# Kernel optimization log

Measured on AMD Instinct MI355X. Metric: run time of the kernel, lower is better.

The kernel has to match this reference:

```python
import jax, jax.numpy as jnp
import numpy as np

CHUNK = 256
THETA = 10000.0

def rope2d(x):
    # x: (b, h, n, d), d divisible by 4
    b, h, n, d = x.shape
    pad = (-n) % CHUNK
    if pad:
        x = jnp.pad(x, ((0, 0), (0, 0), (0, pad), (0, 0)))
    c = (n + pad) // CHUNK
    x = x.reshape(b, h, c, CHUNK, d)
    inv = 1.0 / THETA ** (jnp.arange(0, d, 4, dtype=jnp.float32) / d)  # (d/4,)
    fl = jnp.arange(CHUNK, dtype=jnp.float32)[:, None] * inv[None, :]  # (l, d/4)
    cos_l, sin_l = jnp.cos(fl), jnp.sin(fl)
    fc = jnp.arange(c, dtype=jnp.float32)[:, None] * inv[None, :]      # (c, d/4)
    cos_c, sin_c = jnp.cos(fc)[:, None, :], jnp.sin(fc)[:, None, :]    # (c, 1, d/4)
    x1, x2, x3, x4 = jnp.split(x, 4, axis=-1)
    r1 = x1 * cos_l - x2 * sin_l
    r2 = x1 * sin_l + x2 * cos_l
    r3 = x3 * cos_c - x4 * sin_c
    r4 = x3 * sin_c + x4 * cos_c
    out = jnp.concatenate([r1, r2, r3, r4], axis=-1).reshape(b, h, c * CHUNK, d)
    return out[:, :, :n]


def setup_inputs():
    key = jax.random.key(0)
    ks = jax.random.split(key, 6)
    dim, heads = 512, 8
    b, n = 2, 2048
    s = 0.02
    return {
        'x': jax.random.normal(ks[0], (b, n, dim), dtype=jnp.float32),
        'w_qkv': jax.random.normal(ks[1], (3 * dim, dim), dtype=jnp.float32) * s,
        'b_qkv': jnp.zeros((3 * dim,), dtype=jnp.float32),
        'w_pre': jax.random.normal(ks[2], (heads, heads), dtype=jnp.float32) * 0.3,
        'w_post': jax.random.normal(ks[3], (heads, heads), dtype=jnp.float32) * 0.3,
        'w_out': jax.random.normal(ks[4], (dim, dim), dtype=jnp.float32) * s,
        'b_out': jnp.zeros((dim,), dtype=jnp.float32),
    }


def reference(x, w_qkv, b_qkv, w_pre, w_post, w_out, b_out):
    b, n, dim = x.shape
    heads = w_pre.shape[0]
    d = dim // heads
    scale = d ** -0.5
    qkv = x @ w_qkv.T + b_qkv                      # (b, n, 3*dim)
    q, k, v = jnp.split(qkv, 3, axis=-1)
    def to_heads(t):
        return t.reshape(b, n, heads, d).transpose(0, 2, 1, 3)  # (b, h, n, d)
    q, k, v = to_heads(q), to_heads(k), to_heads(v)
    q = rope2d(q)
    k = rope2d(k)
    logits = jnp.einsum('bhid,bhjd->bhij', q, k) * scale
    # talking-heads pre-softmax mix (Linear over head dim, no bias)
    logits = jnp.einsum('bhij,gh->bgij', logits, w_pre)
    attn = jax.nn.softmax(logits, axis=-1)
    # post-softmax mix
    attn = jnp.einsum('bhij,gh->bgij', attn, w_post)
    out = jnp.einsum('bhij,bhjd->bhid', attn, v)   # (b, h, n, d)
    out = out.transpose(0, 2, 1, 3).reshape(b, n, dim)
    return out @ w_out.T + b_out
```

## Files before the change

kernel.cpp:

```cpp
#include <hip/hip_runtime.h>
#include <hip/hip_bf16.h>

typedef __attribute__((ext_vector_type(8))) short bf16x8;
typedef __attribute__((ext_vector_type(4))) float f32x4;

#define DEV static __device__ __forceinline__

DEV unsigned short f2bf(float f) {
    __hip_bfloat16 h = __float2bfloat16(f);
    return __builtin_bit_cast(unsigned short, h);
}
DEV float bf2f(unsigned short s) {
    union { unsigned int u; float f; } v; v.u = ((unsigned int)s) << 16; return v.f;
}
DEV bf16x8 ld_bf8(const unsigned short* p) { return *reinterpret_cast<const bf16x8*>(p); }
DEV f32x4 mfma16(bf16x8 a, bf16x8 b, f32x4 c) {
    return __builtin_amdgcn_mfma_f32_16x16x32_bf16(a, b, c, 0, 0, 0);
}
DEV bf16x8 make_wfrag(const float* wmat, int li, int lg, float scale) {
    bf16x8 f = {};
    if (lg == 0 && li < 8) {
        #pragma unroll
        for (int t = 0; t < 8; t++) f[t] = (short)f2bf(wmat[li*8 + t] * scale);
    }
    return f;
}

__global__ __launch_bounds__(256) void k_qkv(
    const float* __restrict__ xf, const float* __restrict__ wf,
    const float* __restrict__ bias,
    unsigned short* __restrict__ Qb, unsigned short* __restrict__ Kb,
    unsigned short* __restrict__ Vt)
{
    __shared__ unsigned short As[64][40];
    __shared__ unsigned short Bs[64][40];
    const int m0 = blockIdx.x * 64, c0 = blockIdx.y * 64;
    const int t = threadIdx.x;
    const int w = t >> 6, lane = t & 63, li = lane & 15, lg = lane >> 4;
    const int wr = w >> 1, wc = w & 1;
    f32x4 acc[2][2] = {};
    const int srow = t >> 2, spart = (t & 3) * 8;
    for (int kt = 0; kt < 512; kt += 32) {
        const float* xs = &xf[(size_t)(m0 + srow) * 512 + kt + spart];
        float4 a0 = *(const float4*)xs, a1 = *(const float4*)(xs + 4);
        const float* wsrc = &wf[(size_t)(c0 + srow) * 512 + kt + spart];
        float4 b0 = *(const float4*)wsrc, b1 = *(const float4*)(wsrc + 4);
        ushort4 ua0 = { f2bf(a0.x), f2bf(a0.y), f2bf(a0.z), f2bf(a0.w) };
        ushort4 ua1 = { f2bf(a1.x), f2bf(a1.y), f2bf(a1.z), f2bf(a1.w) };
        ushort4 ub0 = { f2bf(b0.x), f2bf(b0.y), f2bf(b0.z), f2bf(b0.w) };
        ushort4 ub1 = { f2bf(b1.x), f2bf(b1.y), f2bf(b1.z), f2bf(b1.w) };
        *(ushort4*)&As[srow][spart] = ua0; *(ushort4*)&As[srow][spart + 4] = ua1;
        *(ushort4*)&Bs[srow][spart] = ub0; *(ushort4*)&Bs[srow][spart + 4] = ub1;
        __syncthreads();
        bf16x8 af[2], bfr[2];
        #pragma unroll
        for (int mf = 0; mf < 2; mf++) af[mf] = ld_bf8(&As[wr*32 + mf*16 + li][lg*8]);
        #pragma unroll
        for (int nf = 0; nf < 2; nf++) bfr[nf] = ld_bf8(&Bs[wc*32 + nf*16 + li][lg*8]);
        #pragma unroll
        for (int mf = 0; mf < 2; mf++)
            #pragma unroll
            for (int nf = 0; nf < 2; nf++)
                acc[mf][nf] = mfma16(af[mf], bfr[nf], acc[mf][nf]);
        __syncthreads();
    }
    const int type = c0 >> 9;
    const int head = (c0 & 511) >> 6;
    const float b0s = bias[c0 + wc*32 + li];
    const float b1s = bias[c0 + wc*32 + 16 + li];
    float invf = 0.f;
    if (type < 2) invf = powf(10000.f, -(float)li * (1.f/16.f));
    #pragma unroll
    for (int mf = 0; mf < 2; mf++) {
        #pragma unroll
        for (int r = 0; r < 4; r++) {
            int grow = m0 + wr*32 + mf*16 + lg*4 + r;
            int tok = grow & 2047, bb = grow >> 11;
            float v0 = acc[mf][0][r] + b0s;
            float v1 = acc[mf][1][r] + b1s;
            if (type < 2) {
                float ang = (wc == 0 ? (float)(tok & 255) : (float)(tok >> 8)) * invf;
                float s, c;
                sincosf(ang, &s, &c);
                float r0 = v0 * c - v1 * s;
                float r1 = v0 * s + v1 * c;
                unsigned short* dst = (type == 0 ? Qb : Kb);
                size_t base = (((size_t)(bb*8 + head)) * 2048 + tok) * 64 + wc*32 + li;
                dst[base]      = f2bf(r0);
                dst[base + 16] = f2bf(r1);
            } else {
                size_t base = (((size_t)(bb*8 + head)) * 64 + wc*32 + li) * 2048 + tok;
                Vt[base]             = f2bf(v0);
                Vt[base + 16 * 2048] = f2bf(v1);
            }
        }
    }
}

#define JC(x) (jh*1024 + ((x) > 15 ? 15 : (x))*64)

#define LOADK(JX) do { const int j0_ = (JX); \
    _Pragma("unroll") for (int nf = 0; nf < 4; nf++) { \
        const unsigned short* kp_ = Kp + (size_t)(j0_ + nf*16 + li) * 64; \
        kf[nf*2]   = ld_bf8(kp_ + lg*8); \
        kf[nf*2+1] = ld_bf8(kp_ + 32 + lg*8); } \
} while (0)

#define LOADV(JX) do { const int j0_ = (JX); \
    _Pragma("unroll") for (int nf = 0; nf < 4; nf++) { \
        const unsigned short* vp_ = Vp + (size_t)(nf*16 + li) * 2048 + j0_; \
        vf[nf*2]   = ld_bf8(vp_ + lg*8); \
        vf[nf*2+1] = ld_bf8(vp_ + 32 + lg*8); } \
} while (0)

#define QKW(LTW) do { \
    f32x4 sq0 = {}, sq1 = {}, sq2 = {}, sq3 = {}; \
    sq0 = mfma16(qa0, kf[0], sq0); sq0 = mfma16(qa1, kf[1], sq0); \
    sq1 = mfma16(qa0, kf[2], sq1); sq1 = mfma16(qa1, kf[3], sq1); \
    sq2 = mfma16(qa0, kf[4], sq2); sq2 = mfma16(qa1, kf[5], sq2); \
    sq3 = mfma16(qa0, kf[6], sq3); sq3 = mfma16(qa1, kf[7], sq3); \
    _Pragma("unroll") for (int r = 0; r < 4; r++) { \
        LTW[((lg*4 + r)*64 +  0 + li)*8 + w] = f2bf(sq0[r]); \
        LTW[((lg*4 + r)*64 + 16 + li)*8 + w] = f2bf(sq1[r]); \
        LTW[((lg*4 + r)*64 + 32 + li)*8 + w] = f2bf(sq2[r]); \
        LTW[((lg*4 + r)*64 + 48 + li)*8 + w] = f2bf(sq3[r]); } \
} while (0)

#define MIX(LTR) do { \
    _Pragma("unroll") for (int x = 0; x < 2; x++) { \
        const int i2 = 2*w + x; f32x4 invl = x ? invlB : invlA; \
        _Pragma("unroll") for (int jj = 0; jj < 4; jj++) { \
            const int e0 = i2*64 + jj*16; \
            bf16x8 bfv = {}; \
            if (lg == 0) bfv = *(const bf16x8*)&LTR[(e0 + li)*8]; \
            f32x4 d = mfma16(W1f, bfv, zero); \
            float p0 = exp2f(d[0]) * invl[0], p1 = exp2f(d[1]) * invl[1]; \
            float p2 = exp2f(d[2]) * invl[2], p3 = exp2f(d[3]) * invl[3]; \
            unsigned lo = (unsigned)f2bf(p0) | ((unsigned)f2bf(p1) << 16); \
            unsigned hi = (unsigned)f2bf(p2) | ((unsigned)f2bf(p3) << 16); \
            unsigned plo = (unsigned)__shfl_xor((int)lo, 16); \
            unsigned phi = (unsigned)__shfl_xor((int)hi, 16); \
            union { unsigned u[4]; bf16x8 v; } af_; \
            af_.u[0] = lo; af_.u[1] = hi; af_.u[2] = plo; af_.u[3] = phi; \
            f32x4 a2 = mfma16(af_.v, W2f, zero); \
            if (li < 8) { \
                ushort4 o = { f2bf(a2[0]), f2bf(a2[1]), f2bf(a2[2]), f2bf(a2[3]) }; \
                *(ushort4*)&Ah[li*1168 + i2*72 + jj*16 + lg*4] = o; } \
        } } \
} while (0)

#define PVOP() do { \
    _Pragma("unroll") for (int kk = 0; kk < 2; kk++) { \
        bf16x8 pa = *(const bf16x8*)&Ah[w*1168 + li*72 + kk*32 + lg*8]; \
        oacc[0] = mfma16(pa, vf[0 + kk], oacc[0]); \
        oacc[1] = mfma16(pa, vf[2 + kk], oacc[1]); \
        oacc[2] = mfma16(pa, vf[4 + kk], oacc[2]); \
        oacc[3] = mfma16(pa, vf[6 + kk], oacc[3]); } \
} while (0)

#define SUMEXP(LTR) do { \
    _Pragma("unroll") for (int x = 0; x < 2; x++) { \
        const int i2 = 2*w + x; float s_ = 0.f; \
        _Pragma("unroll") for (int jj = 0; jj < 4; jj++) { \
            const int e0 = i2*64 + jj*16; \
            bf16x8 bfv = {}; \
            if (lg == 0) bfv = *(const bf16x8*)&LTR[(e0 + li)*8]; \
            f32x4 d = mfma16(bfv, W1f, zero); \
            s_ += (exp2f(d[0]) + exp2f(d[1])) + (exp2f(d[2]) + exp2f(d[3])); } \
        if (x == 0) lacc0 += s_; else lacc1 += s_; } \
} while (0)

__global__ __launch_bounds__(512, 4) void k_lsum(
    const unsigned short* __restrict__ Qb, const unsigned short* __restrict__ Kb,
    const float* __restrict__ w_pre, float* __restrict__ Lp)
{
    __shared__ unsigned short LtA[8192];
    __shared__ unsigned short LtB[8192];
    const int orig = blockIdx.x;
    const int virt = ((orig & 7) << 6) | (orig >> 3);
    const int jh = virt & 1, it = (virt >> 1) & 127, bb = virt >> 8;
    const int i0 = it * 16;
    const int tid = threadIdx.x, w = tid >> 6, lane = tid & 63, li = lane & 15, lg = lane >> 4;
    bf16x8 W1f = make_wfrag(w_pre, li, lg, 0.125f * 1.44269504088896340736f);
    const unsigned short* Qp = Qb + (((size_t)(bb*8 + w)) * 2048 + i0 + li) * 64;
    bf16x8 qa0 = ld_bf8(Qp + lg*8), qa1 = ld_bf8(Qp + 32 + lg*8);
    const unsigned short* Kp = Kb + ((size_t)(bb*8 + w)) * 2048 * 64;
    const f32x4 zero = {};
    bf16x8 kf[8];
    LOADK(JC(0));
    QKW(LtA);
    LOADK(JC(1));
    __syncthreads();
    float lacc0 = 0.f, lacc1 = 0.f;
    #pragma unroll 1
    for (int tt = 0; tt < 8; tt++) {
        QKW(LtB);
        SUMEXP(LtA);
        LOADK(JC(2*tt + 2));
        __syncthreads();
        if (tt < 7) { QKW(LtA); }
        SUMEXP(LtB);
        if (tt < 7) { LOADK(JC(2*tt + 3)); }
        __syncthreads();
    }
    lacc0 += __shfl_xor(lacc0, 16); lacc0 += __shfl_xor(lacc0, 32);
    lacc1 += __shfl_xor(lacc1, 16); lacc1 += __shfl_xor(lacc1, 32);
    if (lg == 0 && li < 8) {
        float* Lpw = Lp + (size_t)jh * 32768;
        size_t base = (size_t)bb*2048 + i0;
        Lpw[(base + 2*w + 0)*8 + li] = lacc0;
        Lpw[(base + 2*w + 1)*8 + li] = lacc1;
    }
}

__global__ __launch_bounds__(512, 4) void k_attn(
    const unsigned short* __restrict__ Qb, const unsigned short* __restrict__ Kb,
    const unsigned short* __restrict__ Vt,
    const float* __restrict__ w_pre, const float* __restrict__ w_post,
    const float* __restrict__ Lp,
    unsigned short* __restrict__ AOp0, unsigned short* __restrict__ AOp1)
{
    __shared__ unsigned short LtA[8192];
    __shared__ unsigned short LtB[8192];
    __shared__ unsigned short Ah[8 * 1168];
    __shared__ float Llds[128];
    const int orig = blockIdx.x;
    const int virt = ((orig & 7) << 6) | (orig >> 3);
    const int jh = virt & 1, it = (virt >> 1) & 127, bb = virt >> 8;
    const int i0 = it * 16;
    const int tid = threadIdx.x, w = tid >> 6, lane = tid & 63, li = lane & 15, lg = lane >> 4;
    bf16x8 W1f = make_wfrag(w_pre, li, lg, 0.125f * 1.44269504088896340736f);
    bf16x8 W2f = make_wfrag(w_post, li, lg, 1.0f);
    if (tid < 128) {
        size_t g = ((size_t)bb*2048 + i0 + (tid >> 3)) * 8 + (tid & 7);
        Llds[tid] = 1.0f / (Lp[g] + Lp[32768 + g]);
    }
    const unsigned short* Qp = Qb + (((size_t)(bb*8 + w)) * 2048 + i0 + li) * 64;
    bf16x8 qa0 = ld_bf8(Qp + lg*8), qa1 = ld_bf8(Qp + 32 + lg*8);
    const unsigned short* Kp = Kb + ((size_t)(bb*8 + w)) * 2048 * 64;
    const unsigned short* Vp = Vt + ((size_t)(bb*8 + w)) * 64 * 2048;
    const f32x4 zero = {};
    bf16x8 kf[8], vf[8];
    LOADK(JC(0));
    LOADV(JC(0));
    QKW(LtA);
    LOADK(JC(1));
    __syncthreads();
    const int lgc = lg & 1;
    f32x4 invlA = *(const f32x4*)&Llds[(2*w + 0)*8 + lgc*4];
    f32x4 invlB = *(const f32x4*)&Llds[(2*w + 1)*8 + lgc*4];
    f32x4 oacc[4] = {};
    #pragma unroll 1
    for (int tt = 0; tt < 8; tt++) {
        QKW(LtB);
        MIX(LtA);
        __syncthreads();
        PVOP();
        LOADV(JC(2*tt + 1));
        LOADK(JC(2*tt + 2));
        __syncthreads();
        if (tt < 7) { QKW(LtA); }
        MIX(LtB);
        __syncthreads();
        PVOP();
        if (tt < 7) { LOADV(JC(2*tt + 2)); LOADK(JC(2*tt + 3)); }
        __syncthreads();
    }
    unsigned short* ao = jh ? AOp1 : AOp0;
    #pragma unroll
    for (int nf = 0; nf < 4; nf++)
        #pragma unroll
        for (int r = 0; r < 4; r++)
            ao[((size_t)bb*2048 + i0 + lg*4 + r)*512 + w*64 + nf*16 + li] = f2bf(oacc[nf][r]);
}

__global__ __launch_bounds__(256) void k_out(
    const unsigned short* __restrict__ a0, const unsigned short* __restrict__ a1,
    const float* __restrict__ wf, const float* __restrict__ bias,
    float* __restrict__ out)
{
    __shared__ unsigned short As[64][40];
    __shared__ unsigned short Bs[64][40];
    const int m0 = blockIdx.x * 64, c0 = blockIdx.y * 64;
    const int t = threadIdx.x;
    const int w = t >> 6, lane = t & 63, li = lane & 15, lg = lane >> 4;
    const int wr = w >> 1, wc = w & 1;
    f32x4 acc[2][2] = {};
    const int srow = t >> 2, spart = (t & 3) * 8;
    for (int kt = 0; kt < 512; kt += 32) {
        size_t aidx = (size_t)(m0 + srow) * 512 + kt + spart;
        uint4 ua = *(const uint4*)&a0[aidx];
        uint4 ub = *(const uint4*)&a1[aidx];
        const unsigned short* pa = (const unsigned short*)&ua;
        const unsigned short* pb = (const unsigned short*)&ub;
        unsigned short us[8];
        #pragma unroll
        for (int q = 0; q < 8; q++) us[q] = f2bf(bf2f(pa[q]) + bf2f(pb[q]));
        *reinterpret_cast<uint4*>(&As[srow][spart]) = *(const uint4*)us;
        const float* wsrc = &wf[(size_t)(c0 + srow) * 512 + kt + spart];
        float4 b0 = *(const float4*)wsrc, b1 = *(const float4*)(wsrc + 4);
        ushort4 ub0 = { f2bf(b0.x), f2bf(b0.y), f2bf(b0.z), f2bf(b0.w) };
        ushort4 ub1 = { f2bf(b1.x), f2bf(b1.y), f2bf(b1.z), f2bf(b1.w) };
        *(ushort4*)&Bs[srow][spart] = ub0; *(ushort4*)&Bs[srow][spart + 4] = ub1;
        __syncthreads();
        bf16x8 af[2], bfr[2];
        #pragma unroll
        for (int mf = 0; mf < 2; mf++) af[mf] = ld_bf8(&As[wr*32 + mf*16 + li][lg*8]);
        #pragma unroll
        for (int nf = 0; nf < 2; nf++) bfr[nf] = ld_bf8(&Bs[wc*32 + nf*16 + li][lg*8]);
        #pragma unroll
        for (int mf = 0; mf < 2; mf++)
            #pragma unroll
            for (int nf = 0; nf < 2; nf++)
                acc[mf][nf] = mfma16(af[mf], bfr[nf], acc[mf][nf]);
        __syncthreads();
    }
    #pragma unroll
    for (int mf = 0; mf < 2; mf++)
        #pragma unroll
        for (int nf = 0; nf < 2; nf++)
            #pragma unroll
            for (int r = 0; r < 4; r++) {
                int grow = m0 + wr*32 + mf*16 + lg*4 + r;
                int gcol = c0 + wc*32 + nf*16 + li;
                out[(size_t)grow * 512 + gcol] = acc[mf][nf][r] + bias[gcol];
            }
}

extern "C" void kernel_launch(void* const* d_in, const int* in_sizes, int n_in,
                              void* d_out, int out_size, void* d_ws, size_t ws_size,
                              hipStream_t stream)
{
    const float* x      = (const float*)d_in[0];
    const float* w_qkv  = (const float*)d_in[1];
    const float* b_qkv  = (const float*)d_in[2];
    const float* w_pre  = (const float*)d_in[3];
    const float* w_post = (const float*)d_in[4];
    const float* w_out  = (const float*)d_in[5];
    const float* b_out  = (const float*)d_in[6];
    float* out = (float*)d_out;

    char* ws = (char*)d_ws;
    unsigned short* Qb   = (unsigned short*)(ws);
    unsigned short* Kb   = (unsigned short*)(ws + 4194304);
    unsigned short* Vt   = (unsigned short*)(ws + 8388608);
    unsigned short* AOp0 = (unsigned short*)(ws + 12582912);
    unsigned short* AOp1 = (unsigned short*)(ws + 16777216);
    float* Lp            = (float*)(ws + 20971520);

    k_qkv<<<dim3(64, 24), 256, 0, stream>>>(x, w_qkv, b_qkv, Qb, Kb, Vt);
    k_lsum<<<512, 512, 0, stream>>>(Qb, Kb, w_pre, Lp);
    k_attn<<<512, 512, 0, stream>>>(Qb, Kb, Vt, w_pre, w_post, Lp, AOp0, AOp1);
    k_out<<<dim3(64, 8), 256, 0, stream>>>(AOp0, AOp1, w_out, b_out, out);
}
```

Measured before the change: 271.3 us.

## Compute all heads per wave and do talking-heads mixing in registers

Reorganizes k_lsum and k_attn so each wave computes QK logits for all 8 heads over its own 16-key slice, with Q staged in LDS. The pre- and post-softmax head mixes then run as scalar FMAs in registers instead of through LDS transposes and small MFMAs. The softmax normalizer becomes a log-sum subtracted inside exp2. This removes the per-element LDS scatter and shuffle traffic of the previous mixing path. In exchange it adds many scalar FMAs per logit, and K/V fragment loads are no longer software-prefetched.

```diff
diff --git a/kernel.cpp b/kernel.cpp
--- a/kernel.cpp
+++ b/kernel.cpp
@@ -16,14 +16,6 @@
 DEV bf16x8 ld_bf8(const unsigned short* p) { return *reinterpret_cast<const bf16x8*>(p); }
 DEV f32x4 mfma16(bf16x8 a, bf16x8 b, f32x4 c) {
     return __builtin_amdgcn_mfma_f32_16x16x32_bf16(a, b, c, 0, 0, 0);
-}
-DEV bf16x8 make_wfrag(const float* wmat, int li, int lg, float scale) {
-    bf16x8 f = {};
-    if (lg == 0 && li < 8) {
-        #pragma unroll
-        for (int t = 0; t < 8; t++) f[t] = (short)f2bf(wmat[li*8 + t] * scale);
-    }
-    return f;
 }
 
 __global__ __launch_bounds__(256) void k_qkv(
@@ -97,119 +89,79 @@
     }
 }
 
-#define JC(x) (jh*1024 + ((x) > 15 ? 15 : (x))*64)
-
-#define LOADK(JX) do { const int j0_ = (JX); \
-    _Pragma("unroll") for (int nf = 0; nf < 4; nf++) { \
-        const unsigned short* kp_ = Kp + (size_t)(j0_ + nf*16 + li) * 64; \
-        kf[nf*2]   = ld_bf8(kp_ + lg*8); \
-        kf[nf*2+1] = ld_bf8(kp_ + 32 + lg*8); } \
+#define SCALE_L2E (0.125f * 1.44269504088896340736f)
+
+#define STAGE_Q() do { \
+    for (int v = threadIdx.x; v < 1024; v += 512) { \
+        int h_ = v >> 7, rest_ = v & 127, i_ = rest_ >> 3, ch_ = rest_ & 7; \
+        *(uint4*)&Qlds[h_][i_][ch_*8] = \
+            *(const uint4*)&Qb[(((size_t)(bb*8 + h_))*2048 + i0 + i_)*64 + ch_*8]; \
+    } \
 } while (0)
 
-#define LOADV(JX) do { const int j0_ = (JX); \
-    _Pragma("unroll") for (int nf = 0; nf < 4; nf++) { \
-        const unsigned short* vp_ = Vp + (size_t)(nf*16 + li) * 2048 + j0_; \
-        vf[nf*2]   = ld_bf8(vp_ + lg*8); \
-        vf[nf*2+1] = ld_bf8(vp_ + 32 + lg*8); } \
-} while (0)
-
-#define QKW(LTW) do { \
-    f32x4 sq0 = {}, sq1 = {}, sq2 = {}, sq3 = {}; \
-    sq0 = mfma16(qa0, kf[0], sq0); sq0 = mfma16(qa1, kf[1], sq0); \
-    sq1 = mfma16(qa0, kf[2], sq1); sq1 = mfma16(qa1, kf[3], sq1); \
-    sq2 = mfma16(qa0, kf[4], sq2); sq2 = mfma16(qa1, kf[5], sq2); \
-    sq3 = mfma16(qa0, kf[6], sq3); sq3 = mfma16(qa1, kf[7], sq3); \
-    _Pragma("unroll") for (int r = 0; r < 4; r++) { \
-        LTW[((lg*4 + r)*64 +  0 + li)*8 + w] = f2bf(sq0[r]); \
-        LTW[((lg*4 + r)*64 + 16 + li)*8 + w] = f2bf(sq1[r]); \
-        LTW[((lg*4 + r)*64 + 32 + li)*8 + w] = f2bf(sq2[r]); \
-        LTW[((lg*4 + r)*64 + 48 + li)*8 + w] = f2bf(sq3[r]); } \
-} while (0)
-
-#define MIX(LTR) do { \
-    _Pragma("unroll") for (int x = 0; x < 2; x++) { \
-        const int i2 = 2*w + x; f32x4 invl = x ? invlB : invlA; \
-        _Pragma("unroll") for (int jj = 0; jj < 4; jj++) { \
-            const int e0 = i2*64 + jj*16; \
-            bf16x8 bfv = {}; \
-            if (lg == 0) bfv = *(const bf16x8*)&LTR[(e0 + li)*8]; \
-            f32x4 d = mfma16(W1f, bfv, zero); \
-            float p0 = exp2f(d[0]) * invl[0], p1 = exp2f(d[1]) * invl[1]; \
-            float p2 = exp2f(d[2]) * invl[2], p3 = exp2f(d[3]) * invl[3]; \
-            unsigned lo = (unsigned)f2bf(p0) | ((unsigned)f2bf(p1) << 16); \
-            unsigned hi = (unsigned)f2bf(p2) | ((unsigned)f2bf(p3) << 16); \
-            unsigned plo = (unsigned)__shfl_xor((int)lo, 16); \
-            unsigned phi = (unsigned)__shfl_xor((int)hi, 16); \
-            union { unsigned u[4]; bf16x8 v; } af_; \
-            af_.u[0] = lo; af_.u[1] = hi; af_.u[2] = plo; af_.u[3] = phi; \
-            f32x4 a2 = mfma16(af_.v, W2f, zero); \
-            if (li < 8) { \
-                ushort4 o = { f2bf(a2[0]), f2bf(a2[1]), f2bf(a2[2]), f2bf(a2[3]) }; \
-                *(ushort4*)&Ah[li*1168 + i2*72 + jj*16 + lg*4] = o; } \
-        } } \
-} while (0)
-
-#define PVOP() do { \
-    _Pragma("unroll") for (int kk = 0; kk < 2; kk++) { \
-        bf16x8 pa = *(const bf16x8*)&Ah[w*1168 + li*72 + kk*32 + lg*8]; \
-        oacc[0] = mfma16(pa, vf[0 + kk], oacc[0]); \
-        oacc[1] = mfma16(pa, vf[2 + kk], oacc[1]); \
-        oacc[2] = mfma16(pa, vf[4 + kk], oacc[2]); \
-        oacc[3] = mfma16(pa, vf[6 + kk], oacc[3]); } \
-} while (0)
-
-#define SUMEXP(LTR) do { \
-    _Pragma("unroll") for (int x = 0; x < 2; x++) { \
-        const int i2 = 2*w + x; float s_ = 0.f; \
-        _Pragma("unroll") for (int jj = 0; jj < 4; jj++) { \
-            const int e0 = i2*64 + jj*16; \
-            bf16x8 bfv = {}; \
-            if (lg == 0) bfv = *(const bf16x8*)&LTR[(e0 + li)*8]; \
-            f32x4 d = mfma16(bfv, W1f, zero); \
-            s_ += (exp2f(d[0]) + exp2f(d[1])) + (exp2f(d[2]) + exp2f(d[3])); } \
-        if (x == 0) lacc0 += s_; else lacc1 += s_; } \
+#define QK_ALLH() do { \
+    _Pragma("unroll") for (int h = 0; h < 8; h++) { \
+        const unsigned short* kp_ = Kb + (((size_t)(bb*8 + h))*2048 + js + li)*64; \
+        bf16x8 k0_ = ld_bf8(kp_ + lg*8), k1_ = ld_bf8(kp_ + 32 + lg*8); \
+        bf16x8 q0_ = ld_bf8(&Qlds[h][li][lg*8]); \
+        bf16x8 q1_ = ld_bf8(&Qlds[h][li][32 + lg*8]); \
+        f32x4 z_ = {}; \
+        z_ = mfma16(q0_, k0_, z_); \
+        acc[h] = mfma16(q1_, k1_, z_); \
+    } \
 } while (0)
 
 __global__ __launch_bounds__(512, 4) void k_lsum(
     const unsigned short* __restrict__ Qb, const unsigned short* __restrict__ Kb,
     const float* __restrict__ w_pre, float* __restrict__ Lp)
 {
-    __shared__ unsigned short LtA[8192];
-    __shared__ unsigned short LtB[8192];
+    __shared__ unsigned short Qlds[8][16][72];
+    __shared__ float Red[8][128];
     const int orig = blockIdx.x;
     const int virt = ((orig & 7) << 6) | (orig >> 3);
     const int jh = virt & 1, it = (virt >> 1) & 127, bb = virt >> 8;
     const int i0 = it * 16;
     const int tid = threadIdx.x, w = tid >> 6, lane = tid & 63, li = lane & 15, lg = lane >> 4;
-    bf16x8 W1f = make_wfrag(w_pre, li, lg, 0.125f * 1.44269504088896340736f);
-    const unsigned short* Qp = Qb + (((size_t)(bb*8 + w)) * 2048 + i0 + li) * 64;
-    bf16x8 qa0 = ld_bf8(Qp + lg*8), qa1 = ld_bf8(Qp + 32 + lg*8);
-    const unsigned short* Kp = Kb + ((size_t)(bb*8 + w)) * 2048 * 64;
-    const f32x4 zero = {};
-    bf16x8 kf[8];
-    LOADK(JC(0));
-    QKW(LtA);
-    LOADK(JC(1));
+    STAGE_Q();
     __syncthreads();
-    float lacc0 = 0.f, lacc1 = 0.f;
+    float lacc[4][8] = {};
     #pragma unroll 1
-    for (int tt = 0; tt < 8; tt++) {
-        QKW(LtB);
-        SUMEXP(LtA);
-        LOADK(JC(2*tt + 2));
-        __syncthreads();
-        if (tt < 7) { QKW(LtA); }
-        SUMEXP(LtB);
-        if (tt < 7) { LOADK(JC(2*tt + 3)); }
-        __syncthreads();
-    }
-    lacc0 += __shfl_xor(lacc0, 16); lacc0 += __shfl_xor(lacc0, 32);
-    lacc1 += __shfl_xor(lacc1, 16); lacc1 += __shfl_xor(lacc1, 32);
-    if (lg == 0 && li < 8) {
+    for (int s = 0; s < 8; s++) {
+        const int js = jh*1024 + s*128 + w*16;
+        f32x4 acc[8];
+        QK_ALLH();
+        #pragma unroll
+        for (int r = 0; r < 4; r++) {
+            #pragma unroll
+            for (int a = 0; a < 8; a++) {
+                float t = 0.f;
+                #pragma unroll
+                for (int h = 0; h < 8; h++) t = fmaf(w_pre[a*8 + h], acc[h][r], t);
+                lacc[r][a] += __builtin_amdgcn_exp2f(t * SCALE_L2E);
+            }
+        }
+    }
+    #pragma unroll
+    for (int m = 1; m <= 8; m <<= 1)
+        #pragma unroll
+        for (int r = 0; r < 4; r++)
+            #pragma unroll
+            for (int a = 0; a < 8; a++)
+                lacc[r][a] += __shfl_xor(lacc[r][a], m);
+    if (li == 0) {
+        #pragma unroll
+        for (int r = 0; r < 4; r++)
+            #pragma unroll
+            for (int a = 0; a < 8; a++)
+                Red[w][(lg*4 + r)*8 + a] = lacc[r][a];
+    }
+    __syncthreads();
+    if (tid < 128) {
+        float s = 0.f;
+        #pragma unroll
+        for (int ww = 0; ww < 8; ww++) s += Red[ww][tid];
         float* Lpw = Lp + (size_t)jh * 32768;
-        size_t base = (size_t)bb*2048 + i0;
-        Lpw[(base + 2*w + 0)*8 + li] = lacc0;
-        Lpw[(base + 2*w + 1)*8 + li] = lacc1;
+        Lpw[((size_t)bb*2048 + i0 + (tid >> 3))*8 + (tid & 7)] = s;
     }
 }
 
@@ -220,51 +172,79 @@
     const float* __restrict__ Lp,
     unsigned short* __restrict__ AOp0, unsigned short* __restrict__ AOp1)
 {
-    __shared__ unsigned short LtA[8192];
-    __shared__ unsigned short LtB[8192];
-    __shared__ unsigned short Ah[8 * 1168];
+    __shared__ unsigned short Qlds[8][16][72];
+    __shared__ unsigned short Ah[8][16][136];
     __shared__ float Llds[128];
     const int orig = blockIdx.x;
     const int virt = ((orig & 7) << 6) | (orig >> 3);
     const int jh = virt & 1, it = (virt >> 1) & 127, bb = virt >> 8;
     const int i0 = it * 16;
     const int tid = threadIdx.x, w = tid >> 6, lane = tid & 63, li = lane & 15, lg = lane >> 4;
-    bf16x8 W1f = make_wfrag(w_pre, li, lg, 0.125f * 1.44269504088896340736f);
-    bf16x8 W2f = make_wfrag(w_post, li, lg, 1.0f);
+    STAGE_Q();
     if (tid < 128) {
-        size_t g = ((size_t)bb*2048 + i0 + (tid >> 3)) * 8 + (tid & 7);
-        Llds[tid] = 1.0f / (Lp[g] + Lp[32768 + g]);
-    }
-    const unsigned short* Qp = Qb + (((size_t)(bb*8 + w)) * 2048 + i0 + li) * 64;
-    bf16x8 qa0 = ld_bf8(Qp + lg*8), qa1 = ld_bf8(Qp + 32 + lg*8);
-    const unsigned short* Kp = Kb + ((size_t)(bb*8 + w)) * 2048 * 64;
+        int i_ = tid >> 3, a_ = tid & 7;
+        size_t g = ((size_t)bb*2048 + i0 + i_)*8 + a_;
+        Llds[a_*16 + i_] = __builtin_amdgcn_logf(Lp[g] + Lp[32768 + g]);
+    }
     const unsigned short* Vp = Vt + ((size_t)(bb*8 + w)) * 64 * 2048;
-    const f32x4 zero = {};
-    bf16x8 kf[8], vf[8];
-    LOADK(JC(0));
-    LOADV(JC(0));
-    QKW(LtA);
-    LOADK(JC(1));
     __syncthreads();
-    const int lgc = lg & 1;
-    f32x4 invlA = *(const f32x4*)&Llds[(2*w + 0)*8 + lgc*4];
-    f32x4 invlB = *(const f32x4*)&Llds[(2*w + 1)*8 + lgc*4];
     f32x4 oacc[4] = {};
     #pragma unroll 1
-    for (int tt = 0; tt < 8; tt++) {
-        QKW(LtB);
-        MIX(LtA);
-        __syncthreads();
-        PVOP();
-        LOADV(JC(2*tt + 1));
-        LOADK(JC(2*tt + 2));
-        __syncthreads();
-        if (tt < 7) { QKW(LtA); }
-        MIX(LtB);
-        __syncthreads();
-        PVOP();
-        if (tt < 7) { LOADV(JC(2*tt + 2)); LOADK(JC(2*tt + 3)); }
-        __syncthreads();
+    for (int s = 0; s < 8; s++) {
+        const int j0 = jh*1024 + s*128;
+        const int js = j0 + w*16;
+        f32x4 acc[8];
+        QK_ALLH();
+        if (s > 0) {
+            const int jp = j0 - 128;
+            #pragma unroll
+            for (int kc = 0; kc < 4; kc++) {
+                bf16x8 pa = ld_bf8(&Ah[w][li][kc*32 + lg*8]);
+                #pragma unroll
+                for (int nf = 0; nf < 4; nf++) {
+                    bf16x8 vfr = ld_bf8(Vp + (size_t)(nf*16 + li)*2048 + jp + kc*32 + lg*8);
+                    oacc[nf] = mfma16(pa, vfr, oacc[nf]);
+                }
+            }
+        }
+        unsigned short a2s[4][8];
+        #pragma unroll
+        for (int r = 0; r < 4; r++) {
+            float p[8];
+            #pragma unroll
+            for (int a = 0; a < 8; a++) {
+                float t = 0.f;
+                #pragma unroll
+                for (int h = 0; h < 8; h++) t = fmaf(w_pre[a*8 + h], acc[h][r], t);
+                p[a] = __builtin_amdgcn_exp2f(t * SCALE_L2E - Llds[a*16 + lg*4 + r]);
+            }
+            #pragma unroll
+            for (int c = 0; c < 8; c++) {
+                float t = 0.f;
+                #pragma unroll
+                for (int a = 0; a < 8; a++) t = fmaf(w_post[c*8 + a], p[a], t);
+                a2s[r][c] = f2bf(t);
+            }
+        }
+        __syncthreads();
+        #pragma unroll
+        for (int r = 0; r < 4; r++)
+            #pragma unroll
+            for (int c = 0; c < 8; c++)
+                Ah[c][lg*4 + r][w*16 + li] = a2s[r][c];
+        __syncthreads();
+    }
+    {
+        const int jp = jh*1024 + 7*128;
+        #pragma unroll
+        for (int kc = 0; kc < 4; kc++) {
+            bf16x8 pa = ld_bf8(&Ah[w][li][kc*32 + lg*8]);
+            #pragma unroll
+            for (int nf = 0; nf < 4; nf++) {
+                bf16x8 vfr = ld_bf8(Vp + (size_t)(nf*16 + li)*2048 + jp + kc*32 + lg*8);
+                oacc[nf] = mfma16(pa, vfr, oacc[nf]);
+            }
+        }
     }
     unsigned short* ao = jh ? AOp1 : AOp0;
     #pragma unroll
```

Result: faster. 247.3 us (-8.9%).
